# Kernel tuning notes

Measured on AMD Instinct MI355X. Metric: run time of the kernel, lower is better.

## Reference

```python
import jax, jax.numpy as jnp
import numpy as np

N_TOKENS = 8192
TOP_K = 2
N_EXPERTS = 8
D_IN = 2048
D_OUT = 2048


def setup_inputs() -> dict:
    key = jax.random.key(0)
    k1, k2, k3, k4 = jax.random.split(key, 4)
    inputs = jax.random.normal(k1, (N_TOKENS, D_IN), dtype=jnp.float32)
    # stored as [E, out, in], matching nn.Parameter(torch.empty(E, output_size, input_size))
    expert_weights = 0.02 * jax.random.normal(k2, (N_EXPERTS, D_OUT, D_IN), dtype=jnp.float32)
    gates = jax.nn.softmax(jax.random.normal(k3, (N_TOKENS, TOP_K), dtype=jnp.float32), axis=-1)
    # per (token, slot) expert assignment, then sort by expert as the router would
    flat_experts = jax.random.randint(k4, (N_TOKENS * TOP_K,), 0, N_EXPERTS, dtype=jnp.int32)
    sorted_scattered_idxs = jnp.argsort(flat_experts).astype(jnp.int32)
    sorted_expert_idxs = flat_experts[sorted_scattered_idxs]
    expert_offsets = jnp.cumsum(jnp.bincount(flat_experts, length=N_EXPERTS)).astype(jnp.int32)
    return {
        "inputs": inputs,
        "expert_weights": expert_weights,
        "gates": gates,
        "k": TOP_K,
        "sorted_expert_idxs": sorted_expert_idxs,
        "sorted_scattered_idxs": sorted_scattered_idxs,
        "expert_offsets": expert_offsets,
    }


def reference(inputs, expert_weights, gates, k, sorted_expert_idxs, sorted_scattered_idxs, expert_offsets):
    N, d_in = inputs.shape
    E = expert_weights.shape[0]
    Nk = N * k
    # forward permutes weight [E, out, in] -> [E, in, out]
    W = jnp.transpose(expert_weights, (0, 2, 1))
    d_out = W.shape[-1]
    # invert the sort: expert id for each flat (token, slot) index
    expert_per_flat = jnp.zeros((Nk,), dtype=sorted_expert_idxs.dtype).at[
        sorted_scattered_idxs].set(sorted_expert_idxs)
    # scatter2scatter: out_flat[j] = x[j // k] @ W[expert_per_flat[j]]
    x_rep = jnp.repeat(inputs, k, axis=0)  # [N*k, d_in]
    out_flat = jnp.zeros((Nk, d_out), dtype=inputs.dtype)
    for e in range(E):  # small fixed expert count; masked grouped GEMM
        mask = (expert_per_flat == e)[:, None]
        out_flat = out_flat + jnp.where(mask, x_rep, 0.0) @ W[e]
    # combine: (gates.unsqueeze(1) @ output_expanded).squeeze(1)
    out = jnp.einsum('nk,nkd->nd', gates, out_flat.reshape(N, k, d_out))
    return out
```

## Files before the change

### kernel.cpp

```cpp
#include <hip/hip_runtime.h>
#include <hip/hip_bf16.h>
#include <stdint.h>

#define NTOK   8192
#define TOPK   2
#define NEXP   8
#define DIN    2048
#define DOUT   2048
#define NK     (NTOK*TOPK)

#define BM 256
#define BN 256
#define BK 32
#define KTILES   (DIN/BK)
#define ABYTES   (BM*BK*2)
#define BBYTES   (BN*BK*2)
#define BUFBYTES (ABYTES+BBYTES)
#define NBUF 4

typedef __bf16 bf16_8 __attribute__((ext_vector_type(8)));
typedef float  f32x4  __attribute__((ext_vector_type(4)));

__device__ __forceinline__ void gl2lds16(const void* g, void* l) {
  auto gp = reinterpret_cast<const __attribute__((address_space(1))) uint32_t*>(
      reinterpret_cast<uintptr_t>(g));
  auto lp = reinterpret_cast<__attribute__((address_space(3))) uint32_t*>(
      reinterpret_cast<uintptr_t>(l));
  __builtin_amdgcn_global_load_lds(gp, lp, 16, 0, 0);
}

__global__ void cvt_all(const float4* __restrict__ w, uint4* __restrict__ wD,
                        const float4* __restrict__ x, uint4* __restrict__ xD,
                        int nW) {
  int b = blockIdx.x;
  const float4* src;
  uint4* dst;
  int i;
  if (b < nW) { src = w; dst = wD; i = b * 256 + threadIdx.x; }
  else        { src = x; dst = xD; i = (b - nW) * 256 + threadIdx.x; }
  float4 a0 = src[2 * i];
  float4 a1 = src[2 * i + 1];
  union { __bf16 h[8]; uint4 u; } r;
  r.h[0] = (__bf16)a0.x; r.h[1] = (__bf16)a0.y; r.h[2] = (__bf16)a0.z; r.h[3] = (__bf16)a0.w;
  r.h[4] = (__bf16)a1.x; r.h[5] = (__bf16)a1.y; r.h[6] = (__bf16)a1.z; r.h[7] = (__bf16)a1.w;
  dst[i] = r.u;
}

__global__ __launch_bounds__(512, 2)
void moe_gemm(const __bf16* __restrict__ X,
              const __bf16* __restrict__ W,
              const int* __restrict__ ssi,
              const int* __restrict__ offs,
              __bf16* __restrict__ flat)
{
  __shared__ char lds[NBUF * BUFBYTES];
  __shared__ int  sTok[BM];
  __shared__ int  sF[BM];

  const int tid = threadIdx.x;
  const int bid = blockIdx.x;
  const int nt  = bid & 7;
  const int mtg = bid >> 3;

  int start = 0, end = 0, e, cum = 0, prev = 0, mloc = 0, found = 0;
  for (e = 0; e < NEXP; ++e) {
    int oe  = offs[e];
    int seg = oe - prev;
    int t   = (seg + BM - 1) >> 8;
    if (mtg < cum + t) { start = prev; end = oe; mloc = mtg - cum; found = 1; break; }
    cum += t; prev = oe;
  }
  if (!found) return;

  const int m0 = start + mloc * BM;

  if (tid < BM) {
    int p     = m0 + tid;
    int valid = p < end;
    int f     = ssi[valid ? p : (end - 1)];
    sTok[tid] = f >> 1;
    sF[tid]   = valid ? f : -1;
  }
  __syncthreads();

  const int rs = tid >> 2;
  const int kc = (tid & 3) ^ ((tid >> 3) & 3);
  const __bf16* pA0 = X + (size_t)sTok[rs]       * DIN + kc * 8;
  const __bf16* pA1 = X + (size_t)sTok[rs + 128] * DIN + kc * 8;
  const __bf16* wBp = W + (size_t)e * DOUT * DIN + (size_t)(nt * BN) * DIN;
  const __bf16* pB0 = wBp + (size_t)rs * DIN + kc * 8;
  const __bf16* pB1 = wBp + (size_t)(rs + 128) * DIN + kc * 8;
  char* wsl = (char*)lds + (tid >> 6) * 1024;

#pragma unroll
  for (int pt = 0; pt < 3; ++pt) {
    char* d = wsl + pt * BUFBYTES;
    gl2lds16(pA0, d);           gl2lds16(pA1, d + 8192);
    gl2lds16(pB0, d + 16384);   gl2lds16(pB1, d + 24576);
    pA0 += BK; pA1 += BK; pB0 += BK; pB1 += BK;
  }

  const int w   = tid >> 6;
  const int l   = tid & 63;
  const int wm  = w >> 2, wn = w & 3;
  const int lr  = l & 15;
  const int kq  = l >> 4;
  const int kqs = kq ^ ((lr >> 1) & 3);
  const char* aBase = (const char*)lds + (wm * 128 + lr) * 64 + kqs * 16;
  const char* bBase = (const char*)lds + ABYTES + (wn * 64 + lr) * 64 + kqs * 16;

  asm volatile("s_waitcnt vmcnt(8)" ::: "memory");
  __builtin_amdgcn_s_barrier();

  f32x4 acc[8][4] = {};
  int rOff = 0;
  int sOff = 3 * BUFBYTES;

  for (int t = 0; t < KTILES; ++t) {
    if (t < KTILES - 3) {
      char* d = wsl + sOff;
      gl2lds16(pA0, d);           gl2lds16(pA1, d + 8192);
      gl2lds16(pB0, d + 16384);   gl2lds16(pB1, d + 24576);
      pA0 += BK; pA1 += BK; pB0 += BK; pB1 += BK;
    }

    const char* aB = aBase + rOff;
    const char* bB = bBase + rOff;
    bf16_8 af[4], bf[4], ag[4];
#pragma unroll
    for (int i = 0; i < 4; ++i) af[i] = *(const bf16_8*)(aB + i * 1024);
#pragma unroll
    for (int i = 0; i < 4; ++i) bf[i] = *(const bf16_8*)(bB + i * 1024);
#pragma unroll
    for (int i = 0; i < 4; ++i) ag[i] = *(const bf16_8*)(aB + 4096 + i * 1024);

    __builtin_amdgcn_s_setprio(1);
#pragma unroll
    for (int am = 0; am < 4; ++am)
#pragma unroll
      for (int bn = 0; bn < 4; ++bn)
        acc[am][bn] = __builtin_amdgcn_mfma_f32_16x16x32_bf16(
            af[am], bf[bn], acc[am][bn], 0, 0, 0);
#pragma unroll
    for (int am = 0; am < 4; ++am)
#pragma unroll
      for (int bn = 0; bn < 4; ++bn)
        acc[am + 4][bn] = __builtin_amdgcn_mfma_f32_16x16x32_bf16(
            ag[am], bf[bn], acc[am + 4][bn], 0, 0, 0);
    __builtin_amdgcn_s_setprio(0);

    if (t < KTILES - 3)       { asm volatile("s_waitcnt vmcnt(8)" ::: "memory"); }
    else if (t == KTILES - 3) { asm volatile("s_waitcnt vmcnt(4)" ::: "memory"); }
    else if (t == KTILES - 2) { asm volatile("s_waitcnt vmcnt(0)" ::: "memory"); }
    if (t < KTILES - 1) __builtin_amdgcn_s_barrier();

    rOff = (rOff + BUFBYTES) & (NBUF * BUFBYTES - 1);
    sOff = (sOff + BUFBYTES) & (NBUF * BUFBYTES - 1);
  }

  const int colBase = nt * BN + wn * 64 + lr;
  const int rq = kq * 4;
#pragma unroll
  for (int am = 0; am < 8; ++am) {
#pragma unroll
    for (int v = 0; v < 4; ++v) {
      int rl = wm * 128 + am * 16 + rq + v;
      int f  = sF[rl];
      if (f < 0) continue;
      __bf16* row = flat + (size_t)f * DOUT + colBase;
#pragma unroll
      for (int bn = 0; bn < 4; ++bn)
        row[bn * 16] = (__bf16)acc[am][bn][v];
    }
  }
}

__global__ __launch_bounds__(256)
void combine(const __bf16* __restrict__ flat, const float* __restrict__ gates,
             float* __restrict__ out) {
  const int n = blockIdx.x;
  const int c = threadIdx.x * 8;
  bf16_8 y0 = *(const bf16_8*)(flat + (size_t)(2 * n)     * DOUT + c);
  bf16_8 y1 = *(const bf16_8*)(flat + (size_t)(2 * n + 1) * DOUT + c);
  const float2 g = *(const float2*)(gates + 2 * n);
  float o[8];
#pragma unroll
  for (int j = 0; j < 8; ++j)
    o[j] = g.x * (float)y0[j] + g.y * (float)y1[j];
  float4* dst = (float4*)(out + (size_t)n * DOUT + c);
  dst[0] = *(float4*)&o[0];
  dst[1] = *(float4*)&o[4];
}

extern "C" void kernel_launch(void* const* d_in, const int* in_sizes, int n_in,
                              void* d_out, int out_size, void* d_ws, size_t ws_size,
                              hipStream_t stream) {
  const float* inputs = (const float*)d_in[0];
  const float* ew     = (const float*)d_in[1];
  const float* gates  = (const float*)d_in[2];
  const int*   ssi    = (const int*)d_in[5];
  const int*   offs   = (const int*)d_in[6];
  float* out = (float*)d_out;

  __bf16* wsW = (__bf16*)d_ws;
  __bf16* wsX = wsW + (size_t)NEXP * DOUT * DIN;
  __bf16* wsF = wsX + (size_t)NTOK * DIN;

  const int n8w = NEXP * DOUT * DIN / 8;
  const int n8x = NTOK * DIN / 8;
  const int nWb = n8w / 256, nXb = n8x / 256;
  cvt_all<<<nWb + nXb, 256, 0, stream>>>((const float4*)ew, (uint4*)wsW,
                                         (const float4*)inputs, (uint4*)wsX, nWb);

  moe_gemm<<<72 * 8, 512, 0, stream>>>(wsX, wsW, ssi, offs, wsF);
  combine<<<NTOK, 256, 0, stream>>>(wsF, gates, out);
}
```

Measured before the change: 448.6 us.

## Switch GEMM to double-buffered LDS and grid-stride conversion/combine kernels

The GEMM drops from a 4-stage LDS ring with 3 tiles in flight to a 2-buffer scheme that waits for all loads before each barrier. It also removes the s_setprio hints and raises launch_bounds min blocks to 4. The cvt_all and combine kernels become fixed 2048-block grid-stride loops instead of one block per chunk. The intent is less LDS per block and fewer launched blocks, at the cost of shallower prefetch, which exposes more memory latency per K tile.

```diff
diff --git a/kernel.cpp b/kernel.cpp
--- a/kernel.cpp
+++ b/kernel.cpp
@@ -14,12 +14,14 @@
 #define BK 32
 #define KTILES   (DIN/BK)
 #define ABYTES   (BM*BK*2)
-#define BBYTES   (BN*BK*2)
-#define BUFBYTES (ABYTES+BBYTES)
-#define NBUF 4
+#define BUFBYTES 32768
+#define NBUF 2
 
 typedef __bf16 bf16_8 __attribute__((ext_vector_type(8)));
 typedef float  f32x4  __attribute__((ext_vector_type(4)));
+
+#define N8W (NEXP*DOUT*DIN/8)
+#define N8X (NTOK*DIN/8)
 
 __device__ __forceinline__ void gl2lds16(const void* g, void* l) {
   auto gp = reinterpret_cast<const __attribute__((address_space(1))) uint32_t*>(
@@ -29,24 +31,26 @@
   __builtin_amdgcn_global_load_lds(gp, lp, 16, 0, 0);
 }
 
-__global__ void cvt_all(const float4* __restrict__ w, uint4* __restrict__ wD,
-                        const float4* __restrict__ x, uint4* __restrict__ xD,
-                        int nW) {
-  int b = blockIdx.x;
-  const float4* src;
-  uint4* dst;
-  int i;
-  if (b < nW) { src = w; dst = wD; i = b * 256 + threadIdx.x; }
-  else        { src = x; dst = xD; i = (b - nW) * 256 + threadIdx.x; }
-  float4 a0 = src[2 * i];
-  float4 a1 = src[2 * i + 1];
-  union { __bf16 h[8]; uint4 u; } r;
-  r.h[0] = (__bf16)a0.x; r.h[1] = (__bf16)a0.y; r.h[2] = (__bf16)a0.z; r.h[3] = (__bf16)a0.w;
-  r.h[4] = (__bf16)a1.x; r.h[5] = (__bf16)a1.y; r.h[6] = (__bf16)a1.z; r.h[7] = (__bf16)a1.w;
-  dst[i] = r.u;
-}
-
-__global__ __launch_bounds__(512, 2)
+__global__ __launch_bounds__(256)
+void cvt_all(const float4* __restrict__ w, uint4* __restrict__ wD,
+             const float4* __restrict__ x, uint4* __restrict__ xD) {
+  const int stride = gridDim.x * blockDim.x;
+  for (int i = blockIdx.x * blockDim.x + threadIdx.x; i < N8W + N8X; i += stride) {
+    const float4* src;
+    uint4* dst;
+    int j;
+    if (i < N8W) { src = w; dst = wD; j = i; }
+    else         { src = x; dst = xD; j = i - N8W; }
+    float4 a0 = src[2 * j];
+    float4 a1 = src[2 * j + 1];
+    union { __bf16 h[8]; uint4 u; } r;
+    r.h[0] = (__bf16)a0.x; r.h[1] = (__bf16)a0.y; r.h[2] = (__bf16)a0.z; r.h[3] = (__bf16)a0.w;
+    r.h[4] = (__bf16)a1.x; r.h[5] = (__bf16)a1.y; r.h[6] = (__bf16)a1.z; r.h[7] = (__bf16)a1.w;
+    dst[j] = r.u;
+  }
+}
+
+__global__ __launch_bounds__(512, 4)
 void moe_gemm(const __bf16* __restrict__ X,
               const __bf16* __restrict__ W,
               const int* __restrict__ ssi,
@@ -92,13 +96,9 @@
   const __bf16* pB1 = wBp + (size_t)(rs + 128) * DIN + kc * 8;
   char* wsl = (char*)lds + (tid >> 6) * 1024;
 
-#pragma unroll
-  for (int pt = 0; pt < 3; ++pt) {
-    char* d = wsl + pt * BUFBYTES;
-    gl2lds16(pA0, d);           gl2lds16(pA1, d + 8192);
-    gl2lds16(pB0, d + 16384);   gl2lds16(pB1, d + 24576);
-    pA0 += BK; pA1 += BK; pB0 += BK; pB1 += BK;
-  }
+  gl2lds16(pA0, wsl);           gl2lds16(pA1, wsl + 8192);
+  gl2lds16(pB0, wsl + 16384);   gl2lds16(pB1, wsl + 24576);
+  pA0 += BK; pA1 += BK; pB0 += BK; pB1 += BK;
 
   const int w   = tid >> 6;
   const int l   = tid & 63;
@@ -109,53 +109,40 @@
   const char* aBase = (const char*)lds + (wm * 128 + lr) * 64 + kqs * 16;
   const char* bBase = (const char*)lds + ABYTES + (wn * 64 + lr) * 64 + kqs * 16;
 
-  asm volatile("s_waitcnt vmcnt(8)" ::: "memory");
+  asm volatile("s_waitcnt vmcnt(0)" ::: "memory");
   __builtin_amdgcn_s_barrier();
 
   f32x4 acc[8][4] = {};
-  int rOff = 0;
-  int sOff = 3 * BUFBYTES;
+  int cur = 0;
 
   for (int t = 0; t < KTILES; ++t) {
-    if (t < KTILES - 3) {
-      char* d = wsl + sOff;
+    if (t < KTILES - 1) {
+      char* d = wsl + (cur ^ 1) * BUFBYTES;
       gl2lds16(pA0, d);           gl2lds16(pA1, d + 8192);
       gl2lds16(pB0, d + 16384);   gl2lds16(pB1, d + 24576);
       pA0 += BK; pA1 += BK; pB0 += BK; pB1 += BK;
     }
 
-    const char* aB = aBase + rOff;
-    const char* bB = bBase + rOff;
-    bf16_8 af[4], bf[4], ag[4];
-#pragma unroll
-    for (int i = 0; i < 4; ++i) af[i] = *(const bf16_8*)(aB + i * 1024);
+    const char* aB = aBase + cur * BUFBYTES;
+    const char* bB = bBase + cur * BUFBYTES;
+    bf16_8 af[8], bf[4];
+#pragma unroll
+    for (int i = 0; i < 8; ++i) af[i] = *(const bf16_8*)(aB + i * 1024);
 #pragma unroll
     for (int i = 0; i < 4; ++i) bf[i] = *(const bf16_8*)(bB + i * 1024);
-#pragma unroll
-    for (int i = 0; i < 4; ++i) ag[i] = *(const bf16_8*)(aB + 4096 + i * 1024);
-
-    __builtin_amdgcn_s_setprio(1);
-#pragma unroll
-    for (int am = 0; am < 4; ++am)
+
+#pragma unroll
+    for (int am = 0; am < 8; ++am)
 #pragma unroll
       for (int bn = 0; bn < 4; ++bn)
         acc[am][bn] = __builtin_amdgcn_mfma_f32_16x16x32_bf16(
             af[am], bf[bn], acc[am][bn], 0, 0, 0);
-#pragma unroll
-    for (int am = 0; am < 4; ++am)
-#pragma unroll
-      for (int bn = 0; bn < 4; ++bn)
-        acc[am + 4][bn] = __builtin_amdgcn_mfma_f32_16x16x32_bf16(
-            ag[am], bf[bn], acc[am + 4][bn], 0, 0, 0);
-    __builtin_amdgcn_s_setprio(0);
-
-    if (t < KTILES - 3)       { asm volatile("s_waitcnt vmcnt(8)" ::: "memory"); }
-    else if (t == KTILES - 3) { asm volatile("s_waitcnt vmcnt(4)" ::: "memory"); }
-    else if (t == KTILES - 2) { asm volatile("s_waitcnt vmcnt(0)" ::: "memory"); }
-    if (t < KTILES - 1) __builtin_amdgcn_s_barrier();
-
-    rOff = (rOff + BUFBYTES) & (NBUF * BUFBYTES - 1);
-    sOff = (sOff + BUFBYTES) & (NBUF * BUFBYTES - 1);
+
+    if (t < KTILES - 1) {
+      asm volatile("s_waitcnt vmcnt(0)" ::: "memory");
+      __builtin_amdgcn_s_barrier();
+      cur ^= 1;
+    }
   }
 
   const int colBase = nt * BN + wn * 64 + lr;
@@ -178,18 +165,22 @@
 __global__ __launch_bounds__(256)
 void combine(const __bf16* __restrict__ flat, const float* __restrict__ gates,
              float* __restrict__ out) {
-  const int n = blockIdx.x;
-  const int c = threadIdx.x * 8;
-  bf16_8 y0 = *(const bf16_8*)(flat + (size_t)(2 * n)     * DOUT + c);
-  bf16_8 y1 = *(const bf16_8*)(flat + (size_t)(2 * n + 1) * DOUT + c);
-  const float2 g = *(const float2*)(gates + 2 * n);
-  float o[8];
-#pragma unroll
-  for (int j = 0; j < 8; ++j)
-    o[j] = g.x * (float)y0[j] + g.y * (float)y1[j];
-  float4* dst = (float4*)(out + (size_t)n * DOUT + c);
-  dst[0] = *(float4*)&o[0];
-  dst[1] = *(float4*)&o[4];
+  const int stride = gridDim.x * blockDim.x;
+  for (int idx = blockIdx.x * blockDim.x + threadIdx.x; idx < NTOK * (DOUT / 8);
+       idx += stride) {
+    const int n = idx >> 8;
+    const int c = (idx & 255) * 8;
+    bf16_8 y0 = *(const bf16_8*)(flat + (size_t)(2 * n)     * DOUT + c);
+    bf16_8 y1 = *(const bf16_8*)(flat + (size_t)(2 * n + 1) * DOUT + c);
+    const float2 g = *(const float2*)(gates + 2 * n);
+    float o[8];
+#pragma unroll
+    for (int j = 0; j < 8; ++j)
+      o[j] = g.x * (float)y0[j] + g.y * (float)y1[j];
+    float4* dst = (float4*)(out + (size_t)n * DOUT + c);
+    dst[0] = *(float4*)&o[0];
+    dst[1] = *(float4*)&o[4];
+  }
 }
 
 extern "C" void kernel_launch(void* const* d_in, const int* in_sizes, int n_in,
@@ -206,12 +197,9 @@
   __bf16* wsX = wsW + (size_t)NEXP * DOUT * DIN;
   __bf16* wsF = wsX + (size_t)NTOK * DIN;
 
-  const int n8w = NEXP * DOUT * DIN / 8;
-  const int n8x = NTOK * DIN / 8;
-  const int nWb = n8w / 256, nXb = n8x / 256;
-  cvt_all<<<nWb + nXb, 256, 0, stream>>>((const float4*)ew, (uint4*)wsW,
-                                         (const float4*)inputs, (uint4*)wsX, nWb);
+  cvt_all<<<2048, 256, 0, stream>>>((const float4*)ew, (uint4*)wsW,
+                                    (const float4*)inputs, (uint4*)wsX);
 
   moe_gemm<<<72 * 8, 512, 0, stream>>>(wsX, wsW, ssi, offs, wsF);
-  combine<<<NTOK, 256, 0, stream>>>(wsF, gates, out);
-}
+  combine<<<2048, 256, 0, stream>>>(wsF, gates, out);
+}
```

Measured after the change: 1.289 ms. +187.4%, slower.
